# Optimization experiments

Hardware: AMD Instinct MI355X
Metric: run time of the kernel (lower is better)

The kernel has to match this reference:

```python
import jax, jax.numpy as jnp
import numpy as np

D_K = 64  # per-head key dim, used for 1/sqrt(d_k) scaling


def setup_inputs() -> dict:
    key = jax.random.key(0)
    ks = jax.random.split(key, 9)
    B, S, D, H, DK, DV = 2, 4096, 512, 8, 64, 64
    s = 0.02
    return {
        "x": jax.random.normal(ks[0], (B, S, D), dtype=jnp.float32),
        "Wq": jax.random.normal(ks[1], (H, D, DK), dtype=jnp.float32) * s,
        "bq": jax.random.normal(ks[2], (H, DK), dtype=jnp.float32) * s,
        "Wk": jax.random.normal(ks[3], (H, D, DK), dtype=jnp.float32) * s,
        "bk": jax.random.normal(ks[4], (H, DK), dtype=jnp.float32) * s,
        "Wv": jax.random.normal(ks[5], (H, D, DV), dtype=jnp.float32) * s,
        "bv": jax.random.normal(ks[6], (H, DV), dtype=jnp.float32) * s,
        "Wo": jax.random.normal(ks[7], (H * DV, D), dtype=jnp.float32) * s,
        "bo": jax.random.normal(ks[8], (D,), dtype=jnp.float32) * s,
    }


def reference(x, Wq, bq, Wk, bk, Wv, bv, Wo, bo):
    # Per-head projections, vectorized over heads: [B,H,S,dk/dv]
    q = jnp.einsum("bsd,hdk->bhsk", x, Wq) + bq[None, :, None, :]
    k = jnp.einsum("bsd,hdk->bhsk", x, Wk) + bk[None, :, None, :]
    v = jnp.einsum("bsd,hdv->bhsv", x, Wv) + bv[None, :, None, :]
    # Scaled dot-product attention (no mask; dropout inactive at eval)
    scores = jnp.einsum("bhsk,bhtk->bhst", q, k) / jnp.sqrt(jnp.float32(D_K))
    attn = jax.nn.softmax(scores, axis=-1)
    o = jnp.einsum("bhst,bhtv->bhsv", attn, v)
    # Concat heads along feature dim: [B,S,H*dv]
    B, H, S, DV = o.shape
    concat = jnp.transpose(o, (0, 2, 1, 3)).reshape(B, S, H * DV)
    return concat @ Wo + bo
```

## Files before the change

kernel.cpp:

```cpp
#include <hip/hip_runtime.h>
#include <hip/hip_bf16.h>

typedef __attribute__((ext_vector_type(8))) short bf16x8;
typedef __attribute__((ext_vector_type(4))) float f32x4;
typedef __attribute__((ext_vector_type(16))) float f32x16;
typedef __attribute__((ext_vector_type(4))) unsigned short u16x4;
typedef __attribute__((ext_vector_type(4))) unsigned int u32x4;

#define NB 2
#define NS 4096
#define ND 512
#define NH 8

__device__ __forceinline__ unsigned short f2bf(float f) {
  unsigned int u = __float_as_uint(f);
  u += 0x7fffu + ((u >> 16) & 1u);
  return (unsigned short)(u >> 16);
}

__device__ __forceinline__ float bf2f(unsigned short h) {
  return __uint_as_float(((unsigned)h) << 16);
}

__device__ __forceinline__ float exp2_hw(float x) {
  float r;
  asm("v_exp_f32 %0, %1" : "=v"(r) : "v"(x));
  return r;
}

__device__ __forceinline__ unsigned cvtpk(float lo, float hi) {
  unsigned r;
  asm("v_cvt_pk_bf16_f32 %0, %1, %2" : "=v"(r) : "v"(lo), "v"(hi));
  return r;
}

__device__ __forceinline__ void swap32(unsigned& a, unsigned& b) {
  asm("v_permlane32_swap_b32 %0, %1" : "+v"(a), "+v"(b));
}

__device__ __forceinline__ bf16x8 mkfrag(unsigned w0, unsigned w1,
                                         unsigned w2, unsigned w3) {
  u32x4 u = {w0, w1, w2, w3};
  return __builtin_bit_cast(bf16x8, u);
}

__device__ __forceinline__ void gload_lds16(const unsigned short* g,
                                            unsigned short* l) {
  __builtin_amdgcn_global_load_lds(
      (const __attribute__((address_space(1))) unsigned int*)g,
      (__attribute__((address_space(3))) unsigned int*)l, 16, 0, 0);
}

__global__ void pack_kernel(const float* __restrict__ x,
                            const float* __restrict__ Wq,
                            const float* __restrict__ Wk,
                            const float* __restrict__ Wv,
                            const float* __restrict__ Wo,
                            unsigned short* __restrict__ x_bf,
                            unsigned short* __restrict__ w3,
                            unsigned short* __restrict__ wo_t)
{
  int idx = blockIdx.x * 256 + threadIdx.x;
  const int NX4 = NB * NS * ND / 4;
  const int NW = 512 * 512;
  if (idx < NX4) {
    const float4 f = ((const float4*)x)[idx];
    u16x4 o;
    o[0] = f2bf(f.x); o[1] = f2bf(f.y); o[2] = f2bf(f.z); o[3] = f2bf(f.w);
    ((u16x4*)x_bf)[idx] = o;
  } else if (idx < NX4 + 3 * NW) {
    int j = idx - NX4;
    int p = j / NW;
    int r = j - p * NW;
    int n = r >> 9, d = r & 511;
    int h = n >> 6, o = n & 63;
    const float* W = (p == 0) ? Wq : (p == 1) ? Wk : Wv;
    w3[j] = f2bf(W[(h * 512 + d) * 64 + o]);
  } else if (idx < NX4 + 4 * NW) {
    int j = idx - NX4 - 3 * NW;
    int n = j >> 9, kk = j & 511;
    wo_t[j] = f2bf(Wo[kk * 512 + n]);
  }
}

template <int MODE>
__global__ __launch_bounds__(256, 2) void gemm_bt(
    const unsigned short* __restrict__ A,
    const unsigned short* __restrict__ Bm,
    const float* __restrict__ b0,
    const float* __restrict__ b1,
    const float* __restrict__ b2,
    unsigned short* __restrict__ qo,
    unsigned short* __restrict__ ko,
    unsigned short* __restrict__ vo,
    float* __restrict__ fo) {
  __shared__ unsigned short Al[2][128 * 32];
  __shared__ unsigned short Bl[2][128 * 32];
  const int t = threadIdx.x;
  const int m0 = blockIdx.x * 128;
  const int n0 = blockIdx.y * 128;
  const int lane = t & 63;
  const int w = t >> 6;
  const int wm = w >> 1, wn = w & 1;
  const int c = lane & 15, g = lane >> 4;

  f32x4 acc[4][4];
#pragma unroll
  for (int i = 0; i < 4; ++i)
#pragma unroll
    for (int j = 0; j < 4; ++j) acc[i][j] = (f32x4){0.f, 0.f, 0.f, 0.f};

  const int rr = lane >> 2;
  const int kc = (lane & 3) * 8;
  const unsigned short* Ab = A + (size_t)(m0 + w * 32 + rr) * 512 + kc;
  const unsigned short* Bb = Bm + (size_t)(n0 + w * 32 + rr) * 512 + kc;

  auto ISSUE = [&](int ks, int bi) {
    const int k0 = ks * 32;
    gload_lds16(Ab + k0, &Al[bi][w * 1024]);
    gload_lds16(Ab + 16 * 512 + k0, &Al[bi][w * 1024 + 512]);
    gload_lds16(Bb + k0, &Bl[bi][w * 1024]);
    gload_lds16(Bb + 16 * 512 + k0, &Bl[bi][w * 1024 + 512]);
  };

  ISSUE(0, 0);
  for (int ks = 0; ks < 16; ++ks) {
    const int cur = ks & 1;
    asm volatile("s_waitcnt vmcnt(0)" ::: "memory");
    __builtin_amdgcn_s_barrier();
    __builtin_amdgcn_sched_barrier(0);
    if (ks + 1 < 16) ISSUE(ks + 1, cur ^ 1);

    bf16x8 af[4], bfr[4];
#pragma unroll
    for (int mf = 0; mf < 4; ++mf)
      af[mf] = *(const bf16x8*)&Al[cur][(wm * 64 + mf * 16 + c) * 32 + g * 8];
#pragma unroll
    for (int nf = 0; nf < 4; ++nf)
      bfr[nf] = *(const bf16x8*)&Bl[cur][(wn * 64 + nf * 16 + c) * 32 + g * 8];
    __builtin_amdgcn_s_setprio(1);
#pragma unroll
    for (int mf = 0; mf < 4; ++mf)
#pragma unroll
      for (int nf = 0; nf < 4; ++nf)
        acc[mf][nf] = __builtin_amdgcn_mfma_f32_16x16x32_bf16(
            af[mf], bfr[nf], acc[mf][nf], 0, 0, 0);
    __builtin_amdgcn_s_setprio(0);
  }

  if (MODE == 0) {
    const int proj = n0 >> 9;
    const float* bias = proj == 0 ? b0 : (proj == 1 ? b1 : b2);
    unsigned short* dst01 = proj == 0 ? qo : ko;
    const float scale = proj == 0 ? 0.18033688011112042f : 1.0f;
#pragma unroll
    for (int nf = 0; nf < 4; ++nf) {
      const int col5 = (n0 + wn * 64 + nf * 16 + c) & 511;
      const int h = col5 >> 6, o = col5 & 63;
      const float bb = bias[col5];
#pragma unroll
      for (int mf = 0; mf < 4; ++mf) {
#pragma unroll
        for (int r = 0; r < 4; ++r) {
          const int m = m0 + wm * 64 + mf * 16 + g * 4 + r;
          const int b = m >> 12, s = m & 4095;
          const unsigned short hb = f2bf((acc[mf][nf][r] + bb) * scale);
          if (proj < 2)
            dst01[((size_t)((b * NH + h) * NS + s)) * 64 + o] = hb;
          else
            vo[((size_t)((b * NH + h) * 64 + o)) * NS + s] = hb;
        }
      }
    }
  } else {
#pragma unroll
    for (int nf = 0; nf < 4; ++nf) {
      const int col = n0 + wn * 64 + nf * 16 + c;
      const float bb = b0[col];
#pragma unroll
      for (int mf = 0; mf < 4; ++mf) {
#pragma unroll
        for (int r = 0; r < 4; ++r) {
          const int m = m0 + wm * 64 + mf * 16 + g * 4 + r;
          fo[(size_t)m * 512 + col] = acc[mf][nf][r] + bb;
        }
      }
    }
  }
}

template <int SPLITS>
__global__ __launch_bounds__(256, 2) void attn_kernel(
    const unsigned short* __restrict__ q,
    const unsigned short* __restrict__ k,
    const unsigned short* __restrict__ vt,
    unsigned short* __restrict__ cc,
    unsigned short* __restrict__ op,
    float* __restrict__ ml)
{
  union SMemU {
    struct { unsigned short Kl[2][4096]; unsigned short Vl[2][4096]; } kv;
    unsigned short Ol[4][32][68];
  };
  __shared__ SMemU sm;
  const int t = threadIdx.x;
  const int w = t >> 6, lane = t & 63;
  const int col = lane & 31, hi = lane >> 5;
  const int bh = blockIdx.y & 15;
  const int sp = blockIdx.y >> 4;
  const int b = bh >> 3, h = bh & 7;
  const int q0 = blockIdx.x * 128 + w * 32;
  const int kbase = sp * (NS / SPLITS);

  const unsigned short* qh = q + (size_t)bh * NS * 64;
  const unsigned short* kh = k + (size_t)bh * NS * 64;
  const unsigned short* vh = vt + (size_t)bh * 64 * NS;

  bf16x8 qf[4];
#pragma unroll
  for (int c = 0; c < 4; ++c)
    qf[c] = *(const bf16x8*)&qh[(size_t)(q0 + col) * 64 + c * 16 + hi * 8];

  const int rl = lane >> 3, chn = lane & 7;
  const int lk = rl * 64 + ((chn ^ (rl & 7)) << 3);
  const int lv = rl * NS + ((chn ^ (rl & 7)) << 3);

  auto ISSUE = [&](int tile, int bi) {
    const unsigned short* gk = kh + (size_t)(kbase + tile * 64 + w * 16) * 64;
    const unsigned short* gv = vh + (size_t)(w * 16) * NS + kbase + tile * 64;
    gload_lds16(gk + lk, &sm.kv.Kl[bi][w * 1024]);
    gload_lds16(gk + lk + 512, &sm.kv.Kl[bi][w * 1024 + 512]);
    gload_lds16(gv + lv, &sm.kv.Vl[bi][w * 1024]);
    gload_lds16(gv + lv + 8 * NS, &sm.kv.Vl[bi][w * 1024 + 512]);
  };

  f32x16 ot0, ot1;
#pragma unroll
  for (int r = 0; r < 16; ++r) { ot0[r] = 0.f; ot1[r] = 0.f; }
  float l_ = 0.f;

  const int NT = NS / (64 * SPLITS);

  ISSUE(0, 0);

  for (int it = 0; it < NT; ++it) {
    const int cur = it & 1;
    asm volatile("s_waitcnt vmcnt(0)" ::: "memory");
    __builtin_amdgcn_s_barrier();
    __builtin_amdgcn_sched_barrier(0);
    if (it + 1 < NT) ISSUE(it + 1, cur ^ 1);

    bf16x8 kfr[2][4];
#pragma unroll
    for (int c = 0; c < 4; ++c) {
      const int cidx = (((2 * c + hi) ^ (col & 7)) << 3);
      kfr[0][c] = *(const bf16x8*)&sm.kv.Kl[cur][col * 64 + cidx];
      kfr[1][c] = *(const bf16x8*)&sm.kv.Kl[cur][(col + 32) * 64 + cidx];
    }
    f32x16 p0, p1;
#pragma unroll
    for (int r = 0; r < 16; ++r) { p0[r] = 0.f; p1[r] = 0.f; }
    __builtin_amdgcn_s_setprio(1);
#pragma unroll
    for (int c = 0; c < 4; ++c) {
      p0 = __builtin_amdgcn_mfma_f32_32x32x16_bf16(kfr[0][c], qf[c], p0, 0, 0, 0);
      p1 = __builtin_amdgcn_mfma_f32_32x32x16_bf16(kfr[1][c], qf[c], p1, 0, 0, 0);
    }
    __builtin_amdgcn_s_setprio(0);

    bf16x8 vfr[2][4];
#pragma unroll
    for (int ks = 0; ks < 4; ++ks) {
      const int cidx = (((2 * ks + hi) ^ (col & 7)) << 3);
      vfr[0][ks] = *(const bf16x8*)&sm.kv.Vl[cur][col * 64 + cidx];
      vfr[1][ks] = *(const bf16x8*)&sm.kv.Vl[cur][(col + 32) * 64 + cidx];
    }

#pragma unroll
    for (int r = 0; r < 16; ++r) {
      p0[r] = exp2_hw(p0[r]);
      p1[r] = exp2_hw(p1[r]);
    }
    {
      float s[8];
#pragma unroll
      for (int r = 0; r < 8; ++r)
        s[r] = (p0[r] + p0[r + 8]) + (p1[r] + p1[r + 8]);
      float rs =
          ((s[0] + s[1]) + (s[2] + s[3])) + ((s[4] + s[5]) + (s[6] + s[7]));
      rs += __shfl_xor(rs, 32, 64);
      l_ += rs;
    }
    bf16x8 pb[4];
    {
      unsigned g0[8], g1[8];
#pragma unroll
      for (int gg = 0; gg < 8; ++gg) {
        g0[gg] = cvtpk(p0[2 * gg], p0[2 * gg + 1]);
        g1[gg] = cvtpk(p1[2 * gg], p1[2 * gg + 1]);
      }
      unsigned a1, b1, c1, d1;
      a1 = g0[0]; b1 = g0[2]; swap32(a1, b1);
      c1 = g0[1]; d1 = g0[3]; swap32(c1, d1);
      pb[0] = mkfrag(a1, c1, b1, d1);
      a1 = g0[4]; b1 = g0[6]; swap32(a1, b1);
      c1 = g0[5]; d1 = g0[7]; swap32(c1, d1);
      pb[1] = mkfrag(a1, c1, b1, d1);
      a1 = g1[0]; b1 = g1[2]; swap32(a1, b1);
      c1 = g1[1]; d1 = g1[3]; swap32(c1, d1);
      pb[2] = mkfrag(a1, c1, b1, d1);
      a1 = g1[4]; b1 = g1[6]; swap32(a1, b1);
      c1 = g1[5]; d1 = g1[7]; swap32(c1, d1);
      pb[3] = mkfrag(a1, c1, b1, d1);
    }

    __builtin_amdgcn_s_setprio(1);
#pragma unroll
    for (int ks = 0; ks < 4; ++ks) {
      ot0 = __builtin_amdgcn_mfma_f32_32x32x16_bf16(vfr[0][ks], pb[ks], ot0, 0, 0, 0);
      ot1 = __builtin_amdgcn_mfma_f32_32x32x16_bf16(vfr[1][ks], pb[ks], ot1, 0, 0, 0);
    }
    __builtin_amdgcn_s_setprio(0);
  }

  __syncthreads();

  const float inv = (SPLITS == 1) ? (1.0f / l_) : 1.0f;
#pragma unroll
  for (int r = 0; r < 16; ++r) {
    const int dvb = (r & 3) + 8 * (r >> 2) + 4 * hi;
    sm.Ol[w][col][dvb] = f2bf(ot0[r] * inv);
    sm.Ol[w][col][dvb + 32] = f2bf(ot1[r] * inv);
  }
  if (SPLITS > 1 && hi == 0)
    ml[(size_t)(sp * 16 + bh) * NS + q0 + col] = l_;
  asm volatile("s_waitcnt lgkmcnt(0)" ::: "memory");
  const int row = lane >> 1;
#pragma unroll
  for (int p = 0; p < 4; ++p) {
    const int chunk = (lane & 1) + 2 * p;
    bf16x8 vv = *(const bf16x8*)&sm.Ol[w][row][chunk * 8];
    if (SPLITS == 1)
      *(bf16x8*)&cc[((size_t)(b * NS + q0 + row)) * 512 + h * 64 + chunk * 8] =
          vv;
    else
      *(bf16x8*)&op[((size_t)(sp * 16 + bh) * NS + q0 + row) * 64 + chunk * 8] =
          vv;
  }
}

template <int SPLITS>
__global__ void combine_kernel(const unsigned short* __restrict__ op,
                               const float* __restrict__ ml,
                               unsigned short* __restrict__ cc) {
  const int id = blockIdx.x * 256 + threadIdx.x;
  const int chunk = id & 7;
  const int qq = (id >> 3) & 4095;
  const int bh = id >> 15;
  const int b = bh >> 3, h = bh & 7;
  float lsum = 0.f;
#pragma unroll
  for (int sp = 0; sp < SPLITS; ++sp)
    lsum += ml[(size_t)(sp * 16 + bh) * NS + qq];
  const float invl = 1.0f / lsum;
  float acc[8];
#pragma unroll
  for (int j = 0; j < 8; ++j) acc[j] = 0.f;
#pragma unroll
  for (int sp = 0; sp < SPLITS; ++sp) {
    const bf16x8 o =
        *(const bf16x8*)&op[((size_t)(sp * 16 + bh) * NS + qq) * 64 + chunk * 8];
#pragma unroll
    for (int j = 0; j < 8; ++j) acc[j] += bf2f((unsigned short)o[j]);
  }
  bf16x8 out;
#pragma unroll
  for (int j = 0; j < 8; ++j) out[j] = (short)f2bf(acc[j] * invl);
  *(bf16x8*)&cc[((size_t)(b * NS + qq)) * 512 + h * 64 + chunk * 8] = out;
}

extern "C" void kernel_launch(void* const* d_in, const int* in_sizes, int n_in,
                              void* d_out, int out_size, void* d_ws, size_t ws_size,
                              hipStream_t stream) {
  const float* x  = (const float*)d_in[0];
  const float* Wq = (const float*)d_in[1];
  const float* bq = (const float*)d_in[2];
  const float* Wk = (const float*)d_in[3];
  const float* bk = (const float*)d_in[4];
  const float* Wv = (const float*)d_in[5];
  const float* bv = (const float*)d_in[6];
  const float* Wo = (const float*)d_in[7];
  const float* bo = (const float*)d_in[8];

  unsigned char* ws = (unsigned char*)d_ws;
  unsigned short* x_bf = (unsigned short*)(ws);
  unsigned short* w3   = (unsigned short*)(ws + 8388608);
  unsigned short* wo_t = (unsigned short*)(ws + 9961472);
  unsigned short* qb   = (unsigned short*)(ws + 10485760);
  unsigned short* kb   = (unsigned short*)(ws + 18874368);
  unsigned short* vb   = (unsigned short*)(ws + 27262976);
  unsigned short* op   = (unsigned short*)(ws + 35651584);
  unsigned short* cc   = x_bf;

  const size_t need4 = 35651584ull + 4ull * 8388608 + 4ull * 16 * 4096 * 4;
  const size_t need2 = 35651584ull + 2ull * 8388608 + 2ull * 16 * 4096 * 4;

  pack_kernel<<<8192, 256, 0, stream>>>(x, Wq, Wk, Wv, Wo, x_bf, w3, wo_t);
  gemm_bt<0><<<dim3(64, 12), 256, 0, stream>>>(x_bf, w3, bq, bk, bv, qb, kb, vb,
                                               nullptr);
  if (ws_size >= need4) {
    float* mlp = (float*)(ws + 35651584 + 4ull * 8388608);
    attn_kernel<4><<<dim3(32, 64), 256, 0, stream>>>(qb, kb, vb, nullptr, op,
                                                     mlp);
    combine_kernel<4><<<2048, 256, 0, stream>>>(op, mlp, cc);
  } else if (ws_size >= need2) {
    float* mlp = (float*)(ws + 35651584 + 2ull * 8388608);
    attn_kernel<2><<<dim3(32, 32), 256, 0, stream>>>(qb, kb, vb, nullptr, op,
                                                     mlp);
    combine_kernel<2><<<2048, 256, 0, stream>>>(op, mlp, cc);
  } else {
    attn_kernel<1><<<dim3(32, 16), 256, 0, stream>>>(qb, kb, vb, cc, nullptr,
                                                     nullptr);
  }
  gemm_bt<1><<<dim3(64, 4), 256, 0, stream>>>(cc, wo_t, bo, nullptr, nullptr,
                                              nullptr, nullptr, nullptr,
                                              (float*)d_out);
}
```

Baseline: 144.5 us.

## Remove split-KV attention and software-pipeline QK of next tile with PV

Drops the split-KV attention variants and the combine kernel, launching a single full-sequence attention kernel per (batch, head, query tile). Introduces a three-buffer K/V LDS ring so the next tile's QK^T MFMAs are issued alongside the current tile's PV MFMAs, with loads prefetched two tiles ahead. This removes the combine launch and partial-output traffic but cuts the grid to a quarter of the blocks, reducing parallelism across CUs, and increases LDS use.

```diff
diff --git a/kernel.cpp b/kernel.cpp
--- a/kernel.cpp
+++ b/kernel.cpp
@@ -16,10 +16,6 @@
   unsigned int u = __float_as_uint(f);
   u += 0x7fffu + ((u >> 16) & 1u);
   return (unsigned short)(u >> 16);
-}
-
-__device__ __forceinline__ float bf2f(unsigned short h) {
-  return __uint_as_float(((unsigned)h) << 16);
 }
 
 __device__ __forceinline__ float exp2_hw(float x) {
@@ -189,28 +185,23 @@
   }
 }
 
-template <int SPLITS>
 __global__ __launch_bounds__(256, 2) void attn_kernel(
     const unsigned short* __restrict__ q,
     const unsigned short* __restrict__ k,
     const unsigned short* __restrict__ vt,
-    unsigned short* __restrict__ cc,
-    unsigned short* __restrict__ op,
-    float* __restrict__ ml)
+    unsigned short* __restrict__ cc)
 {
   union SMemU {
-    struct { unsigned short Kl[2][4096]; unsigned short Vl[2][4096]; } kv;
+    struct { unsigned short Kl[3][4096]; unsigned short Vl[3][4096]; } kv;
     unsigned short Ol[4][32][68];
   };
   __shared__ SMemU sm;
   const int t = threadIdx.x;
   const int w = t >> 6, lane = t & 63;
   const int col = lane & 31, hi = lane >> 5;
-  const int bh = blockIdx.y & 15;
-  const int sp = blockIdx.y >> 4;
+  const int bh = blockIdx.y;
   const int b = bh >> 3, h = bh & 7;
   const int q0 = blockIdx.x * 128 + w * 32;
-  const int kbase = sp * (NS / SPLITS);
 
   const unsigned short* qh = q + (size_t)bh * NS * 64;
   const unsigned short* kh = k + (size_t)bh * NS * 64;
@@ -226,8 +217,8 @@
   const int lv = rl * NS + ((chn ^ (rl & 7)) << 3);
 
   auto ISSUE = [&](int tile, int bi) {
-    const unsigned short* gk = kh + (size_t)(kbase + tile * 64 + w * 16) * 64;
-    const unsigned short* gv = vh + (size_t)(w * 16) * NS + kbase + tile * 64;
+    const unsigned short* gk = kh + (size_t)(tile * 64 + w * 16) * 64;
+    const unsigned short* gv = vh + (size_t)(w * 16) * NS + tile * 64;
     gload_lds16(gk + lk, &sm.kv.Kl[bi][w * 1024]);
     gload_lds16(gk + lk + 512, &sm.kv.Kl[bi][w * 1024 + 512]);
     gload_lds16(gv + lv, &sm.kv.Vl[bi][w * 1024]);
@@ -239,34 +230,37 @@
   for (int r = 0; r < 16; ++r) { ot0[r] = 0.f; ot1[r] = 0.f; }
   float l_ = 0.f;
 
-  const int NT = NS / (64 * SPLITS);
+  const int NT = NS / 64;
 
   ISSUE(0, 0);
-
-  for (int it = 0; it < NT; ++it) {
-    const int cur = it & 1;
-    asm volatile("s_waitcnt vmcnt(0)" ::: "memory");
-    __builtin_amdgcn_s_barrier();
-    __builtin_amdgcn_sched_barrier(0);
-    if (it + 1 < NT) ISSUE(it + 1, cur ^ 1);
-
-    bf16x8 kfr[2][4];
+  ISSUE(1, 1);
+  asm volatile("s_waitcnt vmcnt(4)" ::: "memory");
+  __builtin_amdgcn_s_barrier();
+  __builtin_amdgcn_sched_barrier(0);
+
+  f32x16 p0, p1;
+  {
+    bf16x8 kfr0[4], kfr1[4];
 #pragma unroll
     for (int c = 0; c < 4; ++c) {
       const int cidx = (((2 * c + hi) ^ (col & 7)) << 3);
-      kfr[0][c] = *(const bf16x8*)&sm.kv.Kl[cur][col * 64 + cidx];
-      kfr[1][c] = *(const bf16x8*)&sm.kv.Kl[cur][(col + 32) * 64 + cidx];
-    }
-    f32x16 p0, p1;
+      kfr0[c] = *(const bf16x8*)&sm.kv.Kl[0][col * 64 + cidx];
+      kfr1[c] = *(const bf16x8*)&sm.kv.Kl[0][(col + 32) * 64 + cidx];
+    }
 #pragma unroll
     for (int r = 0; r < 16; ++r) { p0[r] = 0.f; p1[r] = 0.f; }
     __builtin_amdgcn_s_setprio(1);
 #pragma unroll
     for (int c = 0; c < 4; ++c) {
-      p0 = __builtin_amdgcn_mfma_f32_32x32x16_bf16(kfr[0][c], qf[c], p0, 0, 0, 0);
-      p1 = __builtin_amdgcn_mfma_f32_32x32x16_bf16(kfr[1][c], qf[c], p1, 0, 0, 0);
+      p0 = __builtin_amdgcn_mfma_f32_32x32x16_bf16(kfr0[c], qf[c], p0, 0, 0, 0);
+      p1 = __builtin_amdgcn_mfma_f32_32x32x16_bf16(kfr1[c], qf[c], p1, 0, 0, 0);
     }
     __builtin_amdgcn_s_setprio(0);
+  }
+
+  for (int it = 0; it < NT; ++it) {
+    const int cur = it - (it / 3) * 3;
+    const int nxt = (cur + 1 == 3) ? 0 : cur + 1;
 
     bf16x8 vfr[2][4];
 #pragma unroll
@@ -314,69 +308,62 @@
       pb[3] = mkfrag(a1, c1, b1, d1);
     }
 
-    __builtin_amdgcn_s_setprio(1);
-#pragma unroll
-    for (int ks = 0; ks < 4; ++ks) {
-      ot0 = __builtin_amdgcn_mfma_f32_32x32x16_bf16(vfr[0][ks], pb[ks], ot0, 0, 0, 0);
-      ot1 = __builtin_amdgcn_mfma_f32_32x32x16_bf16(vfr[1][ks], pb[ks], ot1, 0, 0, 0);
-    }
-    __builtin_amdgcn_s_setprio(0);
+    if (it + 1 < NT) {
+      asm volatile("s_waitcnt vmcnt(0)" ::: "memory");
+      __builtin_amdgcn_s_barrier();
+      __builtin_amdgcn_sched_barrier(0);
+      const int b2 = (nxt + 1 == 3) ? 0 : nxt + 1;
+      if (it + 2 < NT) ISSUE(it + 2, b2);
+
+      bf16x8 kfr0[4], kfr1[4];
+#pragma unroll
+      for (int c = 0; c < 4; ++c) {
+        const int cidx = (((2 * c + hi) ^ (col & 7)) << 3);
+        kfr0[c] = *(const bf16x8*)&sm.kv.Kl[nxt][col * 64 + cidx];
+        kfr1[c] = *(const bf16x8*)&sm.kv.Kl[nxt][(col + 32) * 64 + cidx];
+      }
+#pragma unroll
+      for (int r = 0; r < 16; ++r) { p0[r] = 0.f; p1[r] = 0.f; }
+      __builtin_amdgcn_s_setprio(1);
+#pragma unroll
+      for (int c = 0; c < 4; ++c) {
+        p0 = __builtin_amdgcn_mfma_f32_32x32x16_bf16(kfr0[c], qf[c], p0, 0, 0, 0);
+        p1 = __builtin_amdgcn_mfma_f32_32x32x16_bf16(kfr1[c], qf[c], p1, 0, 0, 0);
+      }
+#pragma unroll
+      for (int ks = 0; ks < 4; ++ks) {
+        ot0 = __builtin_amdgcn_mfma_f32_32x32x16_bf16(vfr[0][ks], pb[ks], ot0, 0, 0, 0);
+        ot1 = __builtin_amdgcn_mfma_f32_32x32x16_bf16(vfr[1][ks], pb[ks], ot1, 0, 0, 0);
+      }
+      __builtin_amdgcn_s_setprio(0);
+    } else {
+      __builtin_amdgcn_s_setprio(1);
+#pragma unroll
+      for (int ks = 0; ks < 4; ++ks) {
+        ot0 = __builtin_amdgcn_mfma_f32_32x32x16_bf16(vfr[0][ks], pb[ks], ot0, 0, 0, 0);
+        ot1 = __builtin_amdgcn_mfma_f32_32x32x16_bf16(vfr[1][ks], pb[ks], ot1, 0, 0, 0);
+      }
+      __builtin_amdgcn_s_setprio(0);
+    }
   }
 
   __syncthreads();
 
-  const float inv = (SPLITS == 1) ? (1.0f / l_) : 1.0f;
+  const float inv = 1.0f / l_;
 #pragma unroll
   for (int r = 0; r < 16; ++r) {
     const int dvb = (r & 3) + 8 * (r >> 2) + 4 * hi;
     sm.Ol[w][col][dvb] = f2bf(ot0[r] * inv);
     sm.Ol[w][col][dvb + 32] = f2bf(ot1[r] * inv);
   }
-  if (SPLITS > 1 && hi == 0)
-    ml[(size_t)(sp * 16 + bh) * NS + q0 + col] = l_;
   asm volatile("s_waitcnt lgkmcnt(0)" ::: "memory");
   const int row = lane >> 1;
 #pragma unroll
   for (int p = 0; p < 4; ++p) {
     const int chunk = (lane & 1) + 2 * p;
     bf16x8 vv = *(const bf16x8*)&sm.Ol[w][row][chunk * 8];
-    if (SPLITS == 1)
-      *(bf16x8*)&cc[((size_t)(b * NS + q0 + row)) * 512 + h * 64 + chunk * 8] =
-          vv;
-    else
-      *(bf16x8*)&op[((size_t)(sp * 16 + bh) * NS + q0 + row) * 64 + chunk * 8] =
-          vv;
-  }
-}
-
-template <int SPLITS>
-__global__ void combine_kernel(const unsigned short* __restrict__ op,
-                               const float* __restrict__ ml,
-                               unsigned short* __restrict__ cc) {
-  const int id = blockIdx.x * 256 + threadIdx.x;
-  const int chunk = id & 7;
-  const int qq = (id >> 3) & 4095;
-  const int bh = id >> 15;
-  const int b = bh >> 3, h = bh & 7;
-  float lsum = 0.f;
-#pragma unroll
-  for (int sp = 0; sp < SPLITS; ++sp)
-    lsum += ml[(size_t)(sp * 16 + bh) * NS + qq];
-  const float invl = 1.0f / lsum;
-  float acc[8];
-#pragma unroll
-  for (int j = 0; j < 8; ++j) acc[j] = 0.f;
-#pragma unroll
-  for (int sp = 0; sp < SPLITS; ++sp) {
-    const bf16x8 o =
-        *(const bf16x8*)&op[((size_t)(sp * 16 + bh) * NS + qq) * 64 + chunk * 8];
-#pragma unroll
-    for (int j = 0; j < 8; ++j) acc[j] += bf2f((unsigned short)o[j]);
-  }
-  bf16x8 out;
-#pragma unroll
-  for (int j = 0; j < 8; ++j) out[j] = (short)f2bf(acc[j] * invl);
-  *(bf16x8*)&cc[((size_t)(b * NS + qq)) * 512 + h * 64 + chunk * 8] = out;
+    *(bf16x8*)&cc[((size_t)(b * NS + q0 + row)) * 512 + h * 64 + chunk * 8] = vv;
+  }
 }
 
 extern "C" void kernel_launch(void* const* d_in, const int* in_sizes, int n_in,
@@ -399,29 +386,12 @@
   unsigned short* qb   = (unsigned short*)(ws + 10485760);
   unsigned short* kb   = (unsigned short*)(ws + 18874368);
   unsigned short* vb   = (unsigned short*)(ws + 27262976);
-  unsigned short* op   = (unsigned short*)(ws + 35651584);
   unsigned short* cc   = x_bf;
-
-  const size_t need4 = 35651584ull + 4ull * 8388608 + 4ull * 16 * 4096 * 4;
-  const size_t need2 = 35651584ull + 2ull * 8388608 + 2ull * 16 * 4096 * 4;
 
   pack_kernel<<<8192, 256, 0, stream>>>(x, Wq, Wk, Wv, Wo, x_bf, w3, wo_t);
   gemm_bt<0><<<dim3(64, 12), 256, 0, stream>>>(x_bf, w3, bq, bk, bv, qb, kb, vb,
                                                nullptr);
-  if (ws_size >= need4) {
-    float* mlp = (float*)(ws + 35651584 + 4ull * 8388608);
-    attn_kernel<4><<<dim3(32, 64), 256, 0, stream>>>(qb, kb, vb, nullptr, op,
-                                                     mlp);
-    combine_kernel<4><<<2048, 256, 0, stream>>>(op, mlp, cc);
-  } else if (ws_size >= need2) {
-    float* mlp = (float*)(ws + 35651584 + 2ull * 8388608);
-    attn_kernel<2><<<dim3(32, 32), 256, 0, stream>>>(qb, kb, vb, nullptr, op,
-                                                     mlp);
-    combine_kernel<2><<<2048, 256, 0, stream>>>(op, mlp, cc);
-  } else {
-    attn_kernel<1><<<dim3(32, 16), 256, 0, stream>>>(qb, kb, vb, cc, nullptr,
-                                                     nullptr);
-  }
+  attn_kernel<<<dim3(32, 16), 256, 0, stream>>>(qb, kb, vb, cc);
   gemm_bt<1><<<dim3(64, 4), 256, 0, stream>>>(cc, wo_t, bo, nullptr, nullptr,
                                               nullptr, nullptr, nullptr,
                                               (float*)d_out);
```

New measurement: 136.7 us. -5.4%, faster.
